# Kernel tuning notes

Hardware: AMD Instinct MI355X
Metric: run time of the kernel (lower is better)

Reference implementation:

```python
import jax, jax.numpy as jnp
import numpy as np

B, T, C, H = 2, 2048, 1024, 16
D = C // H  # head dim = 64

def setup_inputs() -> dict:
    key = jax.random.key(0)
    k1, k2, k3 = jax.random.split(key, 3)
    x = jax.random.normal(k1, (B, T, C), dtype=jnp.float32)
    w_attn = jax.random.normal(k2, (C, 3 * C), dtype=jnp.float32) * (1.0 / np.sqrt(C))
    w_proj = jax.random.normal(k3, (C, C), dtype=jnp.float32) * (1.0 / np.sqrt(C))
    return {"x": x, "w_attn": w_attn, "w_proj": w_proj}

def reference(x, w_attn, w_proj):
    # qkv projection: [B,T,3C]
    qkv = jnp.einsum('btc,cd->btd', x, w_attn)
    q, k, v = jnp.split(qkv, 3, axis=-1)
    # reshape to [B,H,T,D]
    q = q.reshape(B, T, H, D).transpose(0, 2, 1, 3)
    k = k.reshape(B, T, H, D).transpose(0, 2, 1, 3)
    v = v.reshape(B, T, H, D).transpose(0, 2, 1, 3)
    scale = 1.0 / jnp.sqrt(jnp.asarray(D, dtype=q.dtype))
    att = jnp.einsum('bhqd,bhkd->bhqk', q, k) * scale  # [B,H,T,T]
    att = jax.nn.softmax(att, axis=-1)
    y = jnp.einsum('bhqk,bhkd->bhqd', att, v)  # [B,H,T,D]
    y = y.transpose(0, 2, 1, 3).reshape(B, T, C)
    return jnp.einsum('btc,cd->btd', y, w_proj)
```

## Files before the change

kernel.cpp:

```cpp
#include <hip/hip_runtime.h>


typedef unsigned short u16;
using bf16x8 = __attribute__((ext_vector_type(8))) short;
using f32x4  = __attribute__((ext_vector_type(4))) float;

#define T_SEQ 2048
#define CDIM  1024

#define QSCALE 0.18033688011112042f

#if __has_builtin(__builtin_amdgcn_exp2f)
#define EXP2(x) __builtin_amdgcn_exp2f(x)
#else
#define EXP2(x) __expf((x) * 0.6931471805599453f)
#endif

__device__ inline u16 f2bf(float f) {
  unsigned int u = __float_as_uint(f);
  u += 0x7FFFu + ((u >> 16) & 1u);
  return (u16)(u >> 16);
}

__device__ inline void gload_lds16(const u16* g, u16* l) {
  __builtin_amdgcn_global_load_lds((const __attribute__((address_space(1))) void*)g,
                                   (__attribute__((address_space(3))) void*)l, 16, 0, 0);
}

__device__ inline int swz128(int r, int c) {
  return (((r << 7) + (c << 1)) ^ ((r & 7) << 4)) >> 1;
}

__global__ __launch_bounds__(256) void conv_bf16_kernel(const float* __restrict__ in,
                                                        u16* __restrict__ out, int n4) {
  int idx = blockIdx.x * 256 + threadIdx.x;
  if (idx >= n4) return;
  float4 v = reinterpret_cast<const float4*>(in)[idx];
  ushort4 o;
  o.x = f2bf(v.x); o.y = f2bf(v.y); o.z = f2bf(v.z); o.w = f2bf(v.w);
  reinterpret_cast<ushort4*>(out)[idx] = o;
}

__global__ __launch_bounds__(256) void transp_conv_kernel(const float* __restrict__ in,
                                                          u16* __restrict__ out, int R, int N,
                                                          int scale_rows, float scale) {
  __shared__ float tile[32][33];
  int nbx = N >> 5;
  int bx = blockIdx.x % nbx, by = blockIdx.x / nbx;
  int tx = threadIdx.x & 31, ty = threadIdx.x >> 5;
#pragma unroll
  for (int rr = ty; rr < 32; rr += 8)
    tile[rr][tx] = in[(long)(by * 32 + rr) * N + bx * 32 + tx];
  __syncthreads();
#pragma unroll
  for (int rr = ty; rr < 32; rr += 8) {
    float s = (bx * 32 + rr) < scale_rows ? scale : 1.0f;
    out[(long)(bx * 32 + rr) * R + by * 32 + tx] = f2bf(tile[tx][rr] * s);
  }
}

template <bool OUT_F32>
__global__ __launch_bounds__(256) void gemm_bt_kernel(const u16* __restrict__ A,
                                                      const u16* __restrict__ Bt,
                                                      void* __restrict__ C,
                                                      int N, int K) {
  __shared__ u16 As[128 * 32];
  __shared__ u16 Bs[128 * 32];
  const int tid = threadIdx.x;
  const int lane = tid & 63, wid = tid >> 6;
  const int l16 = lane & 15, lh = lane >> 4;
  const int wm = wid >> 1, wn = wid & 1;
  const int tm = blockIdx.x & 31;
  const int tn = blockIdx.x >> 5;

  f32x4 acc[4][4];
#pragma unroll
  for (int i = 0; i < 4; ++i)
#pragma unroll
    for (int j = 0; j < 4; ++j)
      acc[i][j] = f32x4{0.f, 0.f, 0.f, 0.f};

  const long aRow = (long)(tm * 128 + wid * 16 + (lane >> 2)) * K + (lane & 3) * 8;
  const long bRow = (long)(tn * 128 + wid * 16 + (lane >> 2)) * K + (lane & 3) * 8;
  const long rstep = (long)64 * K;
  u16* aL = As + wid * 512;
  u16* bL = Bs + wid * 512;

  for (int k0 = 0; k0 < K; k0 += 32) {
    gload_lds16(A + aRow + k0, aL);
    gload_lds16(A + aRow + rstep + k0, aL + 2048);
    gload_lds16(Bt + bRow + k0, bL);
    gload_lds16(Bt + bRow + rstep + k0, bL + 2048);
    __syncthreads();

    bf16x8 af[4], bfr[4];
#pragma unroll
    for (int i = 0; i < 4; ++i)
      af[i] = *reinterpret_cast<const bf16x8*>(&As[(wm * 64 + i * 16 + l16) * 32 + lh * 8]);
#pragma unroll
    for (int j = 0; j < 4; ++j)
      bfr[j] = *reinterpret_cast<const bf16x8*>(&Bs[(wn * 64 + j * 16 + l16) * 32 + lh * 8]);
#pragma unroll
    for (int i = 0; i < 4; ++i)
#pragma unroll
      for (int j = 0; j < 4; ++j)
        acc[i][j] = __builtin_amdgcn_mfma_f32_16x16x32_bf16(af[i], bfr[j], acc[i][j], 0, 0, 0);
    __syncthreads();
  }

#pragma unroll
  for (int i = 0; i < 4; ++i) {
#pragma unroll
    for (int j = 0; j < 4; ++j) {
#pragma unroll
      for (int r = 0; r < 4; ++r) {
        long row = tm * 128 + wm * 64 + i * 16 + lh * 4 + r;
        long col = tn * 128 + wn * 64 + j * 16 + l16;
        if (OUT_F32)
          reinterpret_cast<float*>(C)[row * N + col] = acc[i][j][r];
        else
          reinterpret_cast<u16*>(C)[row * N + col] = f2bf(acc[i][j][r]);
      }
    }
  }
}

__global__ __launch_bounds__(256) void vtrans_kernel(const u16* __restrict__ qkv,
                                                     u16* __restrict__ vT) {
  __shared__ u16 Ts[64 * 64];
  const int tid = threadIdx.x;
  const int bid = blockIdx.x;
  const int tt = bid & 31, bh = bid >> 5;
  const int b = bh >> 4, h = bh & 15;
  const int sr = tid >> 2, sc = (tid & 3) * 16;
  const u16* src = qkv + (long)(b * T_SEQ + tt * 64 + sr) * 3072 + 2 * CDIM + h * 64 + sc;
  uint4 v0 = *reinterpret_cast<const uint4*>(src);
  uint4 v1 = *reinterpret_cast<const uint4*>(src + 8);
  *reinterpret_cast<uint4*>(&Ts[swz128(sr, sc)]) = v0;
  *reinterpret_cast<uint4*>(&Ts[swz128(sr, sc + 8)]) = v1;
  __syncthreads();
  union { uint4 u[2]; u16 s[16]; } o;
#pragma unroll
  for (int i = 0; i < 16; ++i) o.s[i] = Ts[swz128(sc + i, sr)];
  u16* dst = vT + (long)(bh * 64 + sr) * T_SEQ + tt * 64 + sc;
  reinterpret_cast<uint4*>(dst)[0] = o.u[0];
  reinterpret_cast<uint4*>(dst)[1] = o.u[1];
}

__global__ __launch_bounds__(256) void attn_kernel(const u16* __restrict__ qkv,
                                                   const u16* __restrict__ vT,
                                                   u16* __restrict__ y) {
  __shared__ u16 Qs[64 * 64];
  __shared__ u16 Ks[64 * 64];
  __shared__ u16 Vt[64 * 64];
  __shared__ u16 Ps[4][16 * 64];
  const int tid = threadIdx.x;
  const int lane = tid & 63, wid = tid >> 6;
  const int l16 = lane & 15, lh = lane >> 4;
  const int bid = blockIdx.x;
  const int qt = bid & 31, h = (bid >> 5) & 15, b = bid >> 9;

  const u16* qbase = qkv + (long)(b * T_SEQ + qt * 64) * 3072 + h * 64;
  const u16* kbase = qkv + (long)(b * T_SEQ) * 3072 + CDIM + h * 64;
  const u16* vtbase = vT + (long)((b * 16 + h) * 64) * T_SEQ;

  const int sr = tid >> 2, sc = (tid & 3) * 16;

  {
    uint4 v0 = *reinterpret_cast<const uint4*>(qbase + (long)sr * 3072 + sc);
    uint4 v1 = *reinterpret_cast<const uint4*>(qbase + (long)sr * 3072 + sc + 8);
    *reinterpret_cast<uint4*>(&Qs[swz128(sr, sc)]) = v0;
    *reinterpret_cast<uint4*>(&Qs[swz128(sr, sc + 8)]) = v1;
  }
  uint4 kr0 = *reinterpret_cast<const uint4*>(kbase + (long)sr * 3072 + sc);
  uint4 kr1 = *reinterpret_cast<const uint4*>(kbase + (long)sr * 3072 + sc + 8);
  uint4 vr0 = *reinterpret_cast<const uint4*>(vtbase + (long)sr * T_SEQ + sc);
  uint4 vr1 = *reinterpret_cast<const uint4*>(vtbase + (long)sr * T_SEQ + sc + 8);

  __syncthreads();
  bf16x8 qf0 = *reinterpret_cast<const bf16x8*>(&Qs[swz128(wid * 16 + l16, lh * 8)]);
  bf16x8 qf1 = *reinterpret_cast<const bf16x8*>(&Qs[swz128(wid * 16 + l16, 32 + lh * 8)]);

  f32x4 oacc[4];
  float lp[4] = {0.f, 0.f, 0.f, 0.f};
#pragma unroll
  for (int cb = 0; cb < 4; ++cb) oacc[cb] = f32x4{0.f, 0.f, 0.f, 0.f};

  for (int kt = 0; kt < 32; ++kt) {
    *reinterpret_cast<uint4*>(&Ks[swz128(sr, sc)]) = kr0;
    *reinterpret_cast<uint4*>(&Ks[swz128(sr, sc + 8)]) = kr1;
    *reinterpret_cast<uint4*>(&Vt[swz128(sr, sc)]) = vr0;
    *reinterpret_cast<uint4*>(&Vt[swz128(sr, sc + 8)]) = vr1;
    __syncthreads();
    if (kt < 31) {
      const u16* ks = kbase + (long)((kt + 1) * 64 + sr) * 3072 + sc;
      const u16* vs = vtbase + (long)sr * T_SEQ + (kt + 1) * 64 + sc;
      kr0 = *reinterpret_cast<const uint4*>(ks);
      kr1 = *reinterpret_cast<const uint4*>(ks + 8);
      vr0 = *reinterpret_cast<const uint4*>(vs);
      vr1 = *reinterpret_cast<const uint4*>(vs + 8);
    }

    f32x4 sacc[4];
#pragma unroll
    for (int cb = 0; cb < 4; ++cb) {
      sacc[cb] = f32x4{0.f, 0.f, 0.f, 0.f};
      bf16x8 kf0 = *reinterpret_cast<const bf16x8*>(&Ks[swz128(cb * 16 + l16, lh * 8)]);
      bf16x8 kf1 = *reinterpret_cast<const bf16x8*>(&Ks[swz128(cb * 16 + l16, 32 + lh * 8)]);
      sacc[cb] = __builtin_amdgcn_mfma_f32_16x16x32_bf16(qf0, kf0, sacc[cb], 0, 0, 0);
      sacc[cb] = __builtin_amdgcn_mfma_f32_16x16x32_bf16(qf1, kf1, sacc[cb], 0, 0, 0);
    }

    float p[4][4];
#pragma unroll
    for (int cb = 0; cb < 4; ++cb)
#pragma unroll
      for (int r = 0; r < 4; ++r) p[cb][r] = EXP2(sacc[cb][r]);
#pragma unroll
    for (int r = 0; r < 4; ++r)
      lp[r] += (p[0][r] + p[1][r]) + (p[2][r] + p[3][r]);

#pragma unroll
    for (int cb = 0; cb < 4; ++cb)
#pragma unroll
      for (int r = 0; r < 4; ++r)
        Ps[wid][swz128(lh * 4 + r, cb * 16 + l16)] = f2bf(p[cb][r]);

    bf16x8 pf0 = *reinterpret_cast<const bf16x8*>(&Ps[wid][swz128(l16, lh * 8)]);
    bf16x8 pf1 = *reinterpret_cast<const bf16x8*>(&Ps[wid][swz128(l16, 32 + lh * 8)]);

#pragma unroll
    for (int cb = 0; cb < 4; ++cb) {
      bf16x8 vf0 = *reinterpret_cast<const bf16x8*>(&Vt[swz128(cb * 16 + l16, lh * 8)]);
      bf16x8 vf1 = *reinterpret_cast<const bf16x8*>(&Vt[swz128(cb * 16 + l16, 32 + lh * 8)]);
      oacc[cb] = __builtin_amdgcn_mfma_f32_16x16x32_bf16(pf0, vf0, oacc[cb], 0, 0, 0);
      oacc[cb] = __builtin_amdgcn_mfma_f32_16x16x32_bf16(pf1, vf1, oacc[cb], 0, 0, 0);
    }
    __syncthreads();
  }

  float inv[4];
#pragma unroll
  for (int r = 0; r < 4; ++r) {
    float s = lp[r];
    s += __shfl_xor(s, 1);
    s += __shfl_xor(s, 2);
    s += __shfl_xor(s, 4);
    s += __shfl_xor(s, 8);
    inv[r] = __builtin_amdgcn_rcpf(s);
  }
  u16* ybase = y + (long)(b * T_SEQ + qt * 64 + wid * 16) * CDIM + h * 64;
#pragma unroll
  for (int cb = 0; cb < 4; ++cb)
#pragma unroll
    for (int r = 0; r < 4; ++r)
      ybase[(long)(lh * 4 + r) * CDIM + cb * 16 + l16] = f2bf(oacc[cb][r] * inv[r]);
}

extern "C" void kernel_launch(void* const* d_in, const int* in_sizes, int n_in,
                              void* d_out, int out_size, void* d_ws, size_t ws_size,
                              hipStream_t stream) {
  const float* x      = (const float*)d_in[0];
  const float* w_attn = (const float*)d_in[1];
  const float* w_proj = (const float*)d_in[2];

  char* ws = (char*)d_ws;
  u16* xb   = (u16*)(ws + 0);
  u16* wat  = (u16*)(ws + 8388608);
  u16* wpt  = (u16*)(ws + 14680064);
  u16* qkvb = (u16*)(ws + 16777216);
  u16* yb   = (u16*)(ws + 41943040);
  u16* vT   = xb;

  conv_bf16_kernel<<<4096, 256, 0, stream>>>(x, xb, 1048576);
  transp_conv_kernel<<<96 * 32, 256, 0, stream>>>(w_attn, wat, 1024, 3072, 1024, QSCALE);
  transp_conv_kernel<<<32 * 32, 256, 0, stream>>>(w_proj, wpt, 1024, 1024, 0, 1.0f);
  gemm_bt_kernel<false><<<32 * 24, 256, 0, stream>>>(xb, wat, qkvb, 3072, 1024);
  vtrans_kernel<<<32 * 32, 256, 0, stream>>>(qkvb, vT);
  attn_kernel<<<2 * 16 * 32, 256, 0, stream>>>(qkvb, vT, yb);
  gemm_bt_kernel<true><<<32 * 8, 256, 0, stream>>>(yb, wpt, d_out, 1024, 1024);
}
```

Measured before the change: 217.2 us.

## Double-buffer GEMM LDS tiles, hoist swizzle offsets, use library bf16 conversion

The GEMM kernel now ping-pongs two LDS buffers so the global-to-LDS load of the next K slice is issued before the MFMAs on the current one, and one barrier per iteration is dropped. The attention kernel precomputes its swizzled LDS offsets outside the loop instead of recomputing them each iteration. The hand-written float-to-bf16 rounding is replaced by the HIP library conversion. Double buffering doubles GEMM LDS use, which can reduce occupancy. The single remaining barrier per iteration may not order the async global_load_lds writes safely without an explicit vmcnt wait.

```diff
diff --git a/kernel.cpp b/kernel.cpp
--- a/kernel.cpp
+++ b/kernel.cpp
@@ -1,4 +1,5 @@
 #include <hip/hip_runtime.h>
+#include <hip/hip_bf16.h>
 
 
 typedef unsigned short u16;
@@ -17,9 +18,8 @@
 #endif
 
 __device__ inline u16 f2bf(float f) {
-  unsigned int u = __float_as_uint(f);
-  u += 0x7FFFu + ((u >> 16) & 1u);
-  return (u16)(u >> 16);
+  __hip_bfloat16 h = __float2bfloat16(f);
+  return *reinterpret_cast<u16*>(&h);
 }
 
 __device__ inline void gload_lds16(const u16* g, u16* l) {
@@ -64,8 +64,8 @@
                                                       const u16* __restrict__ Bt,
                                                       void* __restrict__ C,
                                                       int N, int K) {
-  __shared__ u16 As[128 * 32];
-  __shared__ u16 Bs[128 * 32];
+  __shared__ u16 As[2][128 * 32];
+  __shared__ u16 Bs[2][128 * 32];
   const int tid = threadIdx.x;
   const int lane = tid & 63, wid = tid >> 6;
   const int l16 = lane & 15, lh = lane >> 4;
@@ -83,29 +83,36 @@
   const long aRow = (long)(tm * 128 + wid * 16 + (lane >> 2)) * K + (lane & 3) * 8;
   const long bRow = (long)(tn * 128 + wid * 16 + (lane >> 2)) * K + (lane & 3) * 8;
   const long rstep = (long)64 * K;
-  u16* aL = As + wid * 512;
-  u16* bL = Bs + wid * 512;
-
+  const int ldsOff = wid * 512;
+
+  gload_lds16(A + aRow, As[0] + ldsOff);
+  gload_lds16(A + aRow + rstep, As[0] + ldsOff + 2048);
+  gload_lds16(Bt + bRow, Bs[0] + ldsOff);
+  gload_lds16(Bt + bRow + rstep, Bs[0] + ldsOff + 2048);
+  __syncthreads();
+
+  int cur = 0;
   for (int k0 = 0; k0 < K; k0 += 32) {
-    gload_lds16(A + aRow + k0, aL);
-    gload_lds16(A + aRow + rstep + k0, aL + 2048);
-    gload_lds16(Bt + bRow + k0, bL);
-    gload_lds16(Bt + bRow + rstep + k0, bL + 2048);
-    __syncthreads();
-
+    if (k0 + 32 < K) {
+      gload_lds16(A + aRow + k0 + 32, As[cur ^ 1] + ldsOff);
+      gload_lds16(A + aRow + rstep + k0 + 32, As[cur ^ 1] + ldsOff + 2048);
+      gload_lds16(Bt + bRow + k0 + 32, Bs[cur ^ 1] + ldsOff);
+      gload_lds16(Bt + bRow + rstep + k0 + 32, Bs[cur ^ 1] + ldsOff + 2048);
+    }
     bf16x8 af[4], bfr[4];
 #pragma unroll
     for (int i = 0; i < 4; ++i)
-      af[i] = *reinterpret_cast<const bf16x8*>(&As[(wm * 64 + i * 16 + l16) * 32 + lh * 8]);
+      af[i] = *reinterpret_cast<const bf16x8*>(&As[cur][(wm * 64 + i * 16 + l16) * 32 + lh * 8]);
 #pragma unroll
     for (int j = 0; j < 4; ++j)
-      bfr[j] = *reinterpret_cast<const bf16x8*>(&Bs[(wn * 64 + j * 16 + l16) * 32 + lh * 8]);
+      bfr[j] = *reinterpret_cast<const bf16x8*>(&Bs[cur][(wn * 64 + j * 16 + l16) * 32 + lh * 8]);
 #pragma unroll
     for (int i = 0; i < 4; ++i)
 #pragma unroll
       for (int j = 0; j < 4; ++j)
         acc[i][j] = __builtin_amdgcn_mfma_f32_16x16x32_bf16(af[i], bfr[j], acc[i][j], 0, 0, 0);
     __syncthreads();
+    cur ^= 1;
   }
 
 #pragma unroll
@@ -165,12 +172,23 @@
   const u16* vtbase = vT + (long)((b * 16 + h) * 64) * T_SEQ;
 
   const int sr = tid >> 2, sc = (tid & 3) * 16;
+  const int ss0 = swz128(sr, sc), ss1 = swz128(sr, sc + 8);
+
+  int kvo[2][4], pwo[4][4];
+#pragma unroll
+  for (int cb = 0; cb < 4; ++cb) {
+    kvo[0][cb] = swz128(cb * 16 + l16, lh * 8);
+    kvo[1][cb] = swz128(cb * 16 + l16, 32 + lh * 8);
+#pragma unroll
+    for (int r = 0; r < 4; ++r) pwo[cb][r] = swz128(lh * 4 + r, cb * 16 + l16);
+  }
+  const int pro0 = swz128(l16, lh * 8), pro1 = swz128(l16, 32 + lh * 8);
 
   {
     uint4 v0 = *reinterpret_cast<const uint4*>(qbase + (long)sr * 3072 + sc);
     uint4 v1 = *reinterpret_cast<const uint4*>(qbase + (long)sr * 3072 + sc + 8);
-    *reinterpret_cast<uint4*>(&Qs[swz128(sr, sc)]) = v0;
-    *reinterpret_cast<uint4*>(&Qs[swz128(sr, sc + 8)]) = v1;
+    *reinterpret_cast<uint4*>(&Qs[ss0]) = v0;
+    *reinterpret_cast<uint4*>(&Qs[ss1]) = v1;
   }
   uint4 kr0 = *reinterpret_cast<const uint4*>(kbase + (long)sr * 3072 + sc);
   uint4 kr1 = *reinterpret_cast<const uint4*>(kbase + (long)sr * 3072 + sc + 8);
@@ -187,10 +205,10 @@
   for (int cb = 0; cb < 4; ++cb) oacc[cb] = f32x4{0.f, 0.f, 0.f, 0.f};
 
   for (int kt = 0; kt < 32; ++kt) {
-    *reinterpret_cast<uint4*>(&Ks[swz128(sr, sc)]) = kr0;
-    *reinterpret_cast<uint4*>(&Ks[swz128(sr, sc + 8)]) = kr1;
-    *reinterpret_cast<uint4*>(&Vt[swz128(sr, sc)]) = vr0;
-    *reinterpret_cast<uint4*>(&Vt[swz128(sr, sc + 8)]) = vr1;
+    *reinterpret_cast<uint4*>(&Ks[ss0]) = kr0;
+    *reinterpret_cast<uint4*>(&Ks[ss1]) = kr1;
+    *reinterpret_cast<uint4*>(&Vt[ss0]) = vr0;
+    *reinterpret_cast<uint4*>(&Vt[ss1]) = vr1;
     __syncthreads();
     if (kt < 31) {
       const u16* ks = kbase + (long)((kt + 1) * 64 + sr) * 3072 + sc;
@@ -205,8 +223,8 @@
 #pragma unroll
     for (int cb = 0; cb < 4; ++cb) {
       sacc[cb] = f32x4{0.f, 0.f, 0.f, 0.f};
-      bf16x8 kf0 = *reinterpret_cast<const bf16x8*>(&Ks[swz128(cb * 16 + l16, lh * 8)]);
-      bf16x8 kf1 = *reinterpret_cast<const bf16x8*>(&Ks[swz128(cb * 16 + l16, 32 + lh * 8)]);
+      bf16x8 kf0 = *reinterpret_cast<const bf16x8*>(&Ks[kvo[0][cb]]);
+      bf16x8 kf1 = *reinterpret_cast<const bf16x8*>(&Ks[kvo[1][cb]]);
       sacc[cb] = __builtin_amdgcn_mfma_f32_16x16x32_bf16(qf0, kf0, sacc[cb], 0, 0, 0);
       sacc[cb] = __builtin_amdgcn_mfma_f32_16x16x32_bf16(qf1, kf1, sacc[cb], 0, 0, 0);
     }
@@ -224,15 +242,15 @@
     for (int cb = 0; cb < 4; ++cb)
 #pragma unroll
       for (int r = 0; r < 4; ++r)
-        Ps[wid][swz128(lh * 4 + r, cb * 16 + l16)] = f2bf(p[cb][r]);
-
-    bf16x8 pf0 = *reinterpret_cast<const bf16x8*>(&Ps[wid][swz128(l16, lh * 8)]);
-    bf16x8 pf1 = *reinterpret_cast<const bf16x8*>(&Ps[wid][swz128(l16, 32 + lh * 8)]);
+        Ps[wid][pwo[cb][r]] = f2bf(p[cb][r]);
+
+    bf16x8 pf0 = *reinterpret_cast<const bf16x8*>(&Ps[wid][pro0]);
+    bf16x8 pf1 = *reinterpret_cast<const bf16x8*>(&Ps[wid][pro1]);
 
 #pragma unroll
     for (int cb = 0; cb < 4; ++cb) {
-      bf16x8 vf0 = *reinterpret_cast<const bf16x8*>(&Vt[swz128(cb * 16 + l16, lh * 8)]);
-      bf16x8 vf1 = *reinterpret_cast<const bf16x8*>(&Vt[swz128(cb * 16 + l16, 32 + lh * 8)]);
+      bf16x8 vf0 = *reinterpret_cast<const bf16x8*>(&Vt[kvo[0][cb]]);
+      bf16x8 vf1 = *reinterpret_cast<const bf16x8*>(&Vt[kvo[1][cb]]);
       oacc[cb] = __builtin_amdgcn_mfma_f32_16x16x32_bf16(pf0, vf0, oacc[cb], 0, 0, 0);
       oacc[cb] = __builtin_amdgcn_mfma_f32_16x16x32_bf16(pf1, vf1, oacc[cb], 0, 0, 0);
     }
```

Result: faster. 205.8 us (-5.3%).
